# Performance work log

Hardware: AMD Instinct MI355X
Metric: run time of the kernel (lower is better)

The kernel has to match this reference:

```python
import jax, jax.numpy as jnp
import numpy as np

B, L, DIM = 16, 1024, 768
HEADS, DIM_HEAD = 12, 64
INNER = HEADS * DIM_HEAD  # 768


def _make_perm(key, l, dim):
    # first `dim` entries identity, rest a random permutation of [dim, l*dim)
    tail = dim + jax.random.permutation(key, (l - 1) * dim)
    return jnp.concatenate([jnp.arange(dim), tail]).astype(jnp.int32)


def setup_inputs() -> dict:
    key = jax.random.key(0)
    kx, kq, kk, kv, ko, kp1, kp2 = jax.random.split(key, 7)
    s = DIM ** -0.5
    return {
        "x": jax.random.normal(kx, (B, L, DIM), dtype=jnp.float32),
        "Wq": jax.random.normal(kq, (DIM, INNER), dtype=jnp.float32) * s,
        "Wk": jax.random.normal(kk, (DIM, INNER), dtype=jnp.float32) * s,
        "Wv": jax.random.normal(kv, (DIM, INNER), dtype=jnp.float32) * s,
        "Wo": jax.random.normal(ko, (INNER, DIM), dtype=jnp.float32) * (INNER ** -0.5),
        "bo": jnp.zeros((DIM,), dtype=jnp.float32),
        "permq": _make_perm(kp1, L, DIM),
        "permk": _make_perm(kp2, L, DIM),
    }


def reference(x, Wq, Wk, Wv, Wo, bo, permq, permk):
    b, l, d = x.shape
    scale = DIM_HEAD ** -0.5
    flat = x.reshape(b, l * d)
    xq = flat[:, permq].reshape(b, l, d)  # irregular gather across (seq*dim)
    xk = flat[:, permk].reshape(b, l, d)
    # projections + head split: b n (h d) -> b h n d
    q = (xq @ Wq).reshape(b, l, HEADS, DIM_HEAD).transpose(0, 2, 1, 3)
    k = (xk @ Wk).reshape(b, l, HEADS, DIM_HEAD).transpose(0, 2, 1, 3)
    v = (x @ Wv).reshape(b, l, HEADS, DIM_HEAD).transpose(0, 2, 1, 3)
    dots = jnp.einsum('bhnd,bhmd->bhnm', q, k) * scale
    attn = jax.nn.softmax(dots, axis=-1)
    out = jnp.einsum('bhnm,bhmd->bhnd', attn, v)
    out = out.transpose(0, 2, 1, 3).reshape(b, l, INNER)
    return out @ Wo + bo
```

## Files before the change

### kernel.cpp

```cpp
#include <hip/hip_runtime.h>

typedef unsigned short u16;
typedef __attribute__((ext_vector_type(8))) short bf16x8;
typedef __attribute__((ext_vector_type(4))) float f32x4;
typedef __attribute__((ext_vector_type(16))) float f32x16;

#define MFMA16(a, b, c) __builtin_amdgcn_mfma_f32_16x16x32_bf16(a, b, c, 0, 0, 0)
#define MFMA32(a, b, c) __builtin_amdgcn_mfma_f32_32x32x16_bf16(a, b, c, 0, 0, 0)

#if defined(__has_builtin)
# if __has_builtin(__builtin_amdgcn_cvt_pk_bf16_f32)
#  define HAS_CVT_PK 1
# else
#  define HAS_CVT_PK 0
# endif
#else
# define HAS_CVT_PK 0
#endif

__device__ __forceinline__ u16 f2b(float f) {
    union { float f; unsigned int u; } v;
    v.f = f;
    unsigned int u = v.u;
    return (u16)((u + 0x7fffu + ((u >> 16) & 1u)) >> 16);
}

__device__ __forceinline__ unsigned int f2b_pk(float a, float b) {
#if HAS_CVT_PK
    auto r = __builtin_amdgcn_cvt_pk_bf16_f32(a, b);
    unsigned int u;
    __builtin_memcpy(&u, &r, 4);
    return u;
#else
    return (unsigned int)f2b(a) | ((unsigned int)f2b(b) << 16);
#endif
}

__device__ __forceinline__ unsigned int cvtpk_asm(float a, float b) {
    unsigned int r;
    asm("v_cvt_pk_bf16_f32 %0, %1, %2" : "=v"(r) : "v"(a), "v"(b));
    return r;
}

__device__ __forceinline__ void g2l16(const u16* gsrc, u16* ldst) {
    __builtin_amdgcn_global_load_lds(
        (const __attribute__((address_space(1))) void*)gsrc,
        (__attribute__((address_space(3))) void*)ldst,
        16, 0, 0);
}

__global__ __launch_bounds__(256) void prep_weights(
    const float* __restrict__ Wq, const float* __restrict__ Wk,
    const float* __restrict__ Wv, const float* __restrict__ Wo,
    u16* __restrict__ wqt, u16* __restrict__ wkt,
    u16* __restrict__ wvt, u16* __restrict__ wot) {
    int id = blockIdx.x * 256 + threadIdx.x;
    int k = id / 768, n = id % 768;
    int t = n * 768 + k;
    wqt[t] = f2b(Wq[id] * (0.125f * 1.44269504088896340736f));
    wkt[t] = f2b(Wk[id]);
    wvt[t] = f2b(Wv[id]);
    wot[t] = f2b(Wo[id]);
}

__global__ __launch_bounds__(256) void cast_transpose(
    const float* __restrict__ x, u16* __restrict__ xb, u16* __restrict__ xT) {
    __shared__ __attribute__((aligned(16))) u16 T[16 * 1032];
    int t = threadIdx.x;
    int j0 = blockIdx.x * 1024;
#pragma unroll
    for (int b = 0; b < 16; ++b) {
        float4 v = *(const float4*)&x[(size_t)b * 786432 + j0 + 4 * t];
        uint2 o = make_uint2(f2b_pk(v.x, v.y), f2b_pk(v.z, v.w));
        *(uint2*)&T[b * 1032 + 4 * t] = o;
        *(uint2*)&xb[(size_t)b * 786432 + j0 + 4 * t] = o;
    }
    __syncthreads();
#pragma unroll
    for (int p = 0; p < 4; ++p) {
        int jl = t + 256 * p;
        union { u16 u[16]; int4 v[2]; } r;
#pragma unroll
        for (int b = 0; b < 16; ++b) r.u[b] = T[b * 1032 + jl];
        size_t base = (size_t)(j0 + jl) * 16;
        *(int4*)&xT[base] = r.v[0];
        *(int4*)&xT[base + 8] = r.v[1];
    }
}

__global__ __launch_bounds__(256) void gather_rows(
    const u16* __restrict__ xT, const int* __restrict__ permq,
    const int* __restrict__ permk, u16* __restrict__ xqT,
    u16* __restrict__ xkT) {
    int j = blockIdx.x * 256 + threadIdx.x;
    int pq = permq[j], pk = permk[j];
    const int4* sq = (const int4*)&xT[(size_t)pq * 16];
    const int4* sk = (const int4*)&xT[(size_t)pk * 16];
    int4 q0 = sq[0], q1 = sq[1];
    int4 k0 = sk[0], k1 = sk[1];
    int4* dq = (int4*)&xqT[(size_t)j * 16];
    int4* dk = (int4*)&xkT[(size_t)j * 16];
    dq[0] = q0; dq[1] = q1;
    dk[0] = k0; dk[1] = k1;
}

__global__ __launch_bounds__(256) void untranspose(
    const u16* __restrict__ srcQ, const u16* __restrict__ srcK,
    u16* __restrict__ dstQ, u16* __restrict__ dstK) {
    __shared__ u16 T[16 * 1034];
    const u16* src = blockIdx.y ? srcK : srcQ;
    u16* dst = blockIdx.y ? dstK : dstQ;
    int t = threadIdx.x;
    int j0 = blockIdx.x * 1024;
#pragma unroll
    for (int p = 0; p < 8; ++p) {
        int c = p * 256 + t;
        union { u16 u[8]; int4 v; } r;
        r.v = *(const int4*)&src[(size_t)j0 * 16 + c * 8];
        int jl = c >> 1, h = (c & 1) * 8;
#pragma unroll
        for (int w = 0; w < 8; ++w) T[(h + w) * 1034 + jl] = r.u[w];
    }
    __syncthreads();
#pragma unroll
    for (int b = 0; b < 16; ++b) {
        const unsigned int* s = (const unsigned int*)&T[b * 1034 + 4 * t];
        uint2 o = make_uint2(s[0], s[1]);
        *(uint2*)&dst[(size_t)b * 786432 + j0 + 4 * t] = o;
    }
}

__device__ __forceinline__ void gemm_core(
    const u16* __restrict__ A, const u16* __restrict__ Bt,
    u16* __restrict__ Cb, float* __restrict__ Cf,
    const float* __restrict__ bias, int m0, int n0, int K, int N, int mode) {
    __shared__ __attribute__((aligned(16))) u16 As[128 * 64];
    __shared__ __attribute__((aligned(16))) u16 Bs[128 * 64];
    int tid = threadIdx.x;
    int wave = tid >> 6, lane = tid & 63;
    int lo = lane & 15, quad = lane >> 4;
    int wm = (wave >> 1) * 64, wn = (wave & 1) * 64;
    f32x4 acc[4][4] = {};

    const u16* pA[4];
    const u16* pB[4];
    u16* lA[4];
    u16* lB[4];
#pragma unroll
    for (int p = 0; p < 4; ++p) {
        int c = p * 256 + wave * 64 + lane;
        int row = c >> 3;
        int scol = ((c & 7) ^ (row & 7)) * 8;
        pA[p] = A + (size_t)(m0 + row) * K + scol;
        pB[p] = Bt + (size_t)(n0 + row) * K + scol;
        lA[p] = &As[(p * 256 + wave * 64) * 8];
        lB[p] = &Bs[(p * 256 + wave * 64) * 8];
    }

    for (int k0 = 0; k0 < K; k0 += 64) {
        __syncthreads();
#pragma unroll
        for (int p = 0; p < 4; ++p) g2l16(pA[p], lA[p]);
#pragma unroll
        for (int p = 0; p < 4; ++p) g2l16(pB[p], lB[p]);
#pragma unroll
        for (int p = 0; p < 4; ++p) { pA[p] += 64; pB[p] += 64; }
        __syncthreads();
#pragma unroll
        for (int kk = 0; kk < 2; ++kk) {
            bf16x8 af[4], bf[4];
#pragma unroll
            for (int mi = 0; mi < 4; ++mi) {
                int row = wm + mi * 16 + lo;
                af[mi] = *(const bf16x8*)&As[row * 64 + (((kk << 2) | quad) ^ (lo & 7)) * 8];
            }
#pragma unroll
            for (int nj = 0; nj < 4; ++nj) {
                int row = wn + nj * 16 + lo;
                bf[nj] = *(const bf16x8*)&Bs[row * 64 + (((kk << 2) | quad) ^ (lo & 7)) * 8];
            }
#pragma unroll
            for (int mi = 0; mi < 4; ++mi)
#pragma unroll
                for (int nj = 0; nj < 4; ++nj)
                    acc[mi][nj] = MFMA16(af[mi], bf[nj], acc[mi][nj]);
        }
    }
#pragma unroll
    for (int mi = 0; mi < 4; ++mi)
#pragma unroll
        for (int nj = 0; nj < 4; ++nj) {
            int col = n0 + wn + nj * 16 + lo;
#pragma unroll
            for (int r = 0; r < 4; ++r) {
                int row = m0 + wm + mi * 16 + quad * 4 + r;
                float v = acc[mi][nj][r];
                if (mode) Cf[(size_t)row * N + col] = v + bias[col];
                else      Cb[(size_t)row * N + col] = f2b(v);
            }
        }
}

__global__ __launch_bounds__(256) void gemm_qkv(
    const u16* __restrict__ xqb, const u16* __restrict__ wqt, u16* __restrict__ Qb,
    const u16* __restrict__ xkb, const u16* __restrict__ wkt, u16* __restrict__ Kb,
    const u16* __restrict__ xb,  const u16* __restrict__ wvt, u16* __restrict__ Vb) {
    int id = blockIdx.x;
    int xcd = id & 7, slot = id >> 3;
    int gi = slot / 6, j = slot % 6;
    int group = xcd + 8 * gi;
    int my = group & 127, z = group >> 7;
    const u16* A = (z == 0) ? xqb : (z == 1) ? xkb : xb;
    const u16* W = (z == 0) ? wqt : (z == 1) ? wkt : wvt;
    u16* C = (z == 0) ? Qb : (z == 1) ? Kb : Vb;
    gemm_core(A, W, C, nullptr, nullptr, my * 128, j * 128, 768, 768, 0);
}

__global__ __launch_bounds__(256) void gemm_out(
    const u16* __restrict__ A, const u16* __restrict__ Bt,
    float* __restrict__ Cf, const float* __restrict__ bias) {
    int id = blockIdx.x;
    int xcd = id & 7, slot = id >> 3;
    int gi = slot / 6, j = slot % 6;
    int group = xcd + 8 * gi;
    gemm_core(A, Bt, nullptr, Cf, bias, group * 128, j * 128, 768, 768, 1);
}

#define LDA 72
__global__ __launch_bounds__(256) void transpose_v(
    const u16* __restrict__ Vb, u16* __restrict__ Vt) {
    __shared__ __attribute__((aligned(16))) u16 tile[64 * LDA];
    int lt = blockIdx.x;
    int bh = blockIdx.y;
    int b = bh / 12, h = bh % 12;
    int tid = threadIdx.x;
    int row = tid >> 3, co = (tid & 7) * 8;
#pragma unroll
    for (int p = 0; p < 2; ++p) {
        int r2 = row + p * 32;
        *(int4*)&tile[r2 * LDA + co] =
            *(const int4*)&Vb[(size_t)(b * 1024 + lt * 64 + r2) * 768 + h * 64 + co];
    }
    __syncthreads();
    int d = tid >> 2, nc = (tid & 3) * 16;
    union { u16 u[16]; int4 v[2]; } tt;
#pragma unroll
    for (int j = 0; j < 16; ++j)
        tt.u[j] = tile[(nc + j) * LDA + d];
    size_t base = ((size_t)bh * 64 + d) * 1024 + lt * 64 + nc;
    *(int4*)&Vt[base] = tt.v[0];
    *(int4*)&Vt[base + 8] = tt.v[1];
}

#define LDK 72
__global__ __launch_bounds__(256) void flash_attn(
    const u16* __restrict__ Qb, const u16* __restrict__ Kb,
    const u16* __restrict__ Vt, u16* __restrict__ AO) {
    __shared__ __attribute__((aligned(16))) u16 Ks[64 * LDK];
    __shared__ __attribute__((aligned(16))) u16 Vs[64 * LDK];
    int id = blockIdx.x;
    int bh = (id & 7) + ((id >> 6) << 3);
    int qt = (id >> 3) & 7;
    int b = bh / 12, h = bh % 12;
    int tid = threadIdx.x, wave = tid >> 6, lane = tid & 63;
    int ln = lane & 31, hi = lane >> 5;
    int q0 = qt * 128;

    bf16x8 qa[4];
    {
        const u16* qrow = &Qb[(size_t)(b * 1024 + q0 + wave * 32 + ln) * 768 + h * 64 + hi * 8];
#pragma unroll
        for (int kk = 0; kk < 4; ++kk)
            qa[kk] = *(const bf16x8*)&qrow[kk * 16];
    }

    const float M2 = 24.0f;
    float l_own = 0.0f;
    f32x16 acc_o[2] = {};
    const size_t kbase = (size_t)b * 1024 * 768 + h * 64;
    const size_t vbase = (size_t)bh * 64 * 1024;
    int srow = tid >> 3, sco = (tid & 7) * 8;

    int4 kr0 = *(const int4*)&Kb[kbase + (size_t)srow * 768 + sco];
    int4 kr1 = *(const int4*)&Kb[kbase + (size_t)(srow + 32) * 768 + sco];
    int4 vr0 = *(const int4*)&Vt[vbase + (size_t)srow * 1024 + sco];
    int4 vr1 = *(const int4*)&Vt[vbase + (size_t)(srow + 32) * 1024 + sco];

    for (int t = 0; t < 16; ++t) {
        __syncthreads();
        *(int4*)&Ks[srow * LDK + sco] = kr0;
        *(int4*)&Ks[(srow + 32) * LDK + sco] = kr1;
        *(int4*)&Vs[srow * LDK + sco] = vr0;
        *(int4*)&Vs[(srow + 32) * LDK + sco] = vr1;
        __syncthreads();
        int tn = (t + 1) & 15;
        kr0 = *(const int4*)&Kb[kbase + (size_t)(tn * 64 + srow) * 768 + sco];
        kr1 = *(const int4*)&Kb[kbase + (size_t)(tn * 64 + srow + 32) * 768 + sco];
        vr0 = *(const int4*)&Vt[vbase + (size_t)srow * 1024 + tn * 64 + sco];
        vr1 = *(const int4*)&Vt[vbase + (size_t)(srow + 32) * 1024 + tn * 64 + sco];
        f32x16 sacc[2] = {};
#pragma unroll
        for (int nj = 0; nj < 2; ++nj)
#pragma unroll
            for (int kk = 0; kk < 4; ++kk) {
                bf16x8 kb = *(const bf16x8*)&Ks[(ln + 32 * nj) * LDK + kk * 16 + hi * 8];
                sacc[nj] = MFMA32(kb, qa[kk], sacc[nj]);
            }
#pragma unroll
        for (int nj = 0; nj < 2; ++nj) {
            float p[16];
#pragma unroll
            for (int r = 0; r < 16; ++r)
                p[r] = __builtin_amdgcn_exp2f(sacc[nj][r] - M2);
            l_own += (((p[0] + p[1]) + (p[2] + p[3])) + ((p[4] + p[5]) + (p[6] + p[7])))
                   + (((p[8] + p[9]) + (p[10] + p[11])) + ((p[12] + p[13]) + (p[14] + p[15])));
            unsigned int c[8];
#pragma unroll
            for (int m = 0; m < 8; ++m)
                c[m] = cvtpk_asm(p[2 * m], p[2 * m + 1]);
            asm("v_permlane32_swap_b32 %0, %1" : "+v"(c[0]), "+v"(c[2]));
            asm("v_permlane32_swap_b32 %0, %1" : "+v"(c[1]), "+v"(c[3]));
            asm("v_permlane32_swap_b32 %0, %1" : "+v"(c[4]), "+v"(c[6]));
            asm("v_permlane32_swap_b32 %0, %1" : "+v"(c[5]), "+v"(c[7]));
            union { unsigned int w[4]; bf16x8 v; } pa0, pa1;
            pa0.w[0] = c[0]; pa0.w[1] = c[1]; pa0.w[2] = c[2]; pa0.w[3] = c[3];
            pa1.w[0] = c[4]; pa1.w[1] = c[5]; pa1.w[2] = c[6]; pa1.w[3] = c[7];
#pragma unroll
            for (int njd = 0; njd < 2; ++njd) {
                bf16x8 vb0 = *(const bf16x8*)&Vs[(ln + 32 * njd) * LDK + (2 * nj) * 16 + hi * 8];
                acc_o[njd] = MFMA32(pa0.v, vb0, acc_o[njd]);
            }
#pragma unroll
            for (int njd = 0; njd < 2; ++njd) {
                bf16x8 vb1 = *(const bf16x8*)&Vs[(ln + 32 * njd) * LDK + (2 * nj + 1) * 16 + hi * 8];
                acc_o[njd] = MFMA32(pa1.v, vb1, acc_o[njd]);
            }
        }
    }
    float l = l_own + __shfl_xor(l_own, 32, 64);
    float inv = 1.0f / l;
#pragma unroll
    for (int r = 0; r < 16; ++r) {
        int qrow = (r & 3) + 8 * (r >> 2) + 4 * hi;
        float invq = __shfl(inv, qrow, 64);
        int row = b * 1024 + q0 + wave * 32 + qrow;
#pragma unroll
        for (int njd = 0; njd < 2; ++njd)
            AO[(size_t)row * 768 + h * 64 + ln + 32 * njd] = f2b(acc_o[njd][r] * invq);
    }
}

static const size_t SZ_W  = (size_t)768 * 768 * 2;
static const size_t SZ_X  = (size_t)16 * 1024 * 768 * 2;
static const size_t OFF_WQT = 0;
static const size_t OFF_WKT = SZ_W;
static const size_t OFF_WVT = 2 * SZ_W;
static const size_t OFF_WOT = 3 * SZ_W;
static const size_t OFF_XB  = 4 * SZ_W;
static const size_t OFF_XQB = OFF_XB  + SZ_X;
static const size_t OFF_XKB = OFF_XQB + SZ_X;
static const size_t OFF_QB  = OFF_XKB + SZ_X;
static const size_t OFF_KB  = OFF_QB  + SZ_X;
static const size_t OFF_VB  = OFF_KB  + SZ_X;
static const size_t OFF_XT  = OFF_QB;
static const size_t OFF_XQT = OFF_KB;
static const size_t OFF_XKT = OFF_VB;
static const size_t OFF_VT  = OFF_XQB;
static const size_t OFF_AO  = OFF_XKB;

extern "C" void kernel_launch(void* const* d_in, const int* in_sizes, int n_in,
                              void* d_out, int out_size, void* d_ws, size_t ws_size,
                              hipStream_t stream) {
    const float* x  = (const float*)d_in[0];
    const float* Wq = (const float*)d_in[1];
    const float* Wk = (const float*)d_in[2];
    const float* Wv = (const float*)d_in[3];
    const float* Wo = (const float*)d_in[4];
    const float* bo = (const float*)d_in[5];
    const int* permq = (const int*)d_in[6];
    const int* permk = (const int*)d_in[7];
    float* out = (float*)d_out;
    char* ws = (char*)d_ws;
    u16* wqt = (u16*)(ws + OFF_WQT);
    u16* wkt = (u16*)(ws + OFF_WKT);
    u16* wvt = (u16*)(ws + OFF_WVT);
    u16* wot = (u16*)(ws + OFF_WOT);
    u16* xb  = (u16*)(ws + OFF_XB);
    u16* xqb = (u16*)(ws + OFF_XQB);
    u16* xkb = (u16*)(ws + OFF_XKB);
    u16* Qb  = (u16*)(ws + OFF_QB);
    u16* Kb  = (u16*)(ws + OFF_KB);
    u16* Vb  = (u16*)(ws + OFF_VB);
    u16* xT  = (u16*)(ws + OFF_XT);
    u16* xqT = (u16*)(ws + OFF_XQT);
    u16* xkT = (u16*)(ws + OFF_XKT);
    u16* Vt  = (u16*)(ws + OFF_VT);
    u16* AO  = (u16*)(ws + OFF_AO);

    prep_weights<<<2304, 256, 0, stream>>>(Wq, Wk, Wv, Wo, wqt, wkt, wvt, wot);
    cast_transpose<<<768, 256, 0, stream>>>(x, xb, xT);
    gather_rows<<<3072, 256, 0, stream>>>(xT, permq, permk, xqT, xkT);
    untranspose<<<dim3(768, 2), 256, 0, stream>>>(xqT, xkT, xqb, xkb);
    gemm_qkv<<<2304, 256, 0, stream>>>(xqb, wqt, Qb, xkb, wkt, Kb, xb, wvt, Vb);
    transpose_v<<<dim3(16, 192), 256, 0, stream>>>(Vb, Vt);
    flash_attn<<<1536, 256, 0, stream>>>(Qb, Kb, Vt, AO);
    gemm_out<<<768, 256, 0, stream>>>(AO, wot, out, bo);
}
```

Measured before the change: 377.4 us.

## Rewrite GEMM core as 256x256 double-buffered tile with 8 waves

Replaces the 128x128 single-buffered GEMM tile (4 waves) with a 256x256 tile computed by 8 waves, LDS double-buffered so global-to-LDS loads for the next K step are issued interleaved with MFMA work on the current buffer. Raw s_barrier plus setprio are used to keep waves in lockstep and prioritize MFMA issue. The aim is more operand reuse per loaded byte and hiding load latency, at the cost of 128KB LDS per block, many more accumulator registers, and far fewer blocks (576 and 192), which may underfill the 256 CUs, especially for gemm_out.

```diff
diff --git a/kernel.cpp b/kernel.cpp
--- a/kernel.cpp
+++ b/kernel.cpp
@@ -130,100 +130,112 @@
     }
 }
 
-__device__ __forceinline__ void gemm_core(
+__device__ __forceinline__ void gemm256_core(
     const u16* __restrict__ A, const u16* __restrict__ Bt,
     u16* __restrict__ Cb, float* __restrict__ Cf,
     const float* __restrict__ bias, int m0, int n0, int K, int N, int mode) {
-    __shared__ __attribute__((aligned(16))) u16 As[128 * 64];
-    __shared__ __attribute__((aligned(16))) u16 Bs[128 * 64];
+    __shared__ __attribute__((aligned(16))) u16 As[2][256 * 64];
+    __shared__ __attribute__((aligned(16))) u16 Bs[2][256 * 64];
     int tid = threadIdx.x;
     int wave = tid >> 6, lane = tid & 63;
+    int wr = wave >> 2, wc = wave & 3;
     int lo = lane & 15, quad = lane >> 4;
-    int wm = (wave >> 1) * 64, wn = (wave & 1) * 64;
-    f32x4 acc[4][4] = {};
-
-    const u16* pA[4];
-    const u16* pB[4];
-    u16* lA[4];
-    u16* lB[4];
-#pragma unroll
-    for (int p = 0; p < 4; ++p) {
-        int c = p * 256 + wave * 64 + lane;
-        int row = c >> 3;
-        int scol = ((c & 7) ^ (row & 7)) * 8;
-        pA[p] = A + (size_t)(m0 + row) * K + scol;
-        pB[p] = Bt + (size_t)(n0 + row) * K + scol;
-        lA[p] = &As[(p * 256 + wave * 64) * 8];
-        lB[p] = &Bs[(p * 256 + wave * 64) * 8];
-    }
-
-    for (int k0 = 0; k0 < K; k0 += 64) {
-        __syncthreads();
-#pragma unroll
-        for (int p = 0; p < 4; ++p) g2l16(pA[p], lA[p]);
-#pragma unroll
-        for (int p = 0; p < 4; ++p) g2l16(pB[p], lB[p]);
-#pragma unroll
-        for (int p = 0; p < 4; ++p) { pA[p] += 64; pB[p] += 64; }
-        __syncthreads();
-#pragma unroll
-        for (int kk = 0; kk < 2; ++kk) {
+    f32x4 acc[8][4] = {};
+
+    const u16* Ab = A + (size_t)m0 * K;
+    const u16* Bb = Bt + (size_t)n0 * K;
+    int r_off = wave * 8 + (lane >> 3);
+    int s_off = ((lane & 7) ^ (lane >> 3)) * 8;
+
+#pragma unroll
+    for (int h = 0; h < 2; ++h)
+#pragma unroll
+        for (int i = 0; i < 2; ++i) {
+            g2l16(Ab + (size_t)(h * 128 + i * 64 + r_off) * K + s_off,
+                  &As[0][(h * 128 + i * 64 + wave * 8) * 64]);
+            g2l16(Bb + (size_t)(h * 128 + i * 64 + r_off) * K + s_off,
+                  &Bs[0][(h * 128 + i * 64 + wave * 8) * 64]);
+        }
+    asm volatile("s_waitcnt vmcnt(0)" ::: "memory");
+    __builtin_amdgcn_s_barrier();
+
+    const int NT = K >> 6;
+    for (int s = 0; s < NT; ++s) {
+        int cur = s & 1, nxt = cur ^ 1;
+        int kn = (s + 1) << 6;
+        const bool more = (s + 1 < NT);
+#pragma unroll
+        for (int q = 0; q < 4; ++q) {
+            const int ks = q >> 1, qm = q & 1;
+            int fs = ((ks * 4 + quad) ^ (lo & 7)) * 8;
             bf16x8 af[4], bf[4];
 #pragma unroll
-            for (int mi = 0; mi < 4; ++mi) {
-                int row = wm + mi * 16 + lo;
-                af[mi] = *(const bf16x8*)&As[row * 64 + (((kk << 2) | quad) ^ (lo & 7)) * 8];
+            for (int mi = 0; mi < 4; ++mi)
+                af[mi] = *(const bf16x8*)&As[cur][(wr * 128 + (qm * 4 + mi) * 16 + lo) * 64 + fs];
+#pragma unroll
+            for (int nj = 0; nj < 4; ++nj)
+                bf[nj] = *(const bf16x8*)&Bs[cur][(wc * 64 + nj * 16 + lo) * 64 + fs];
+            if (more) {
+                const u16* src = (q < 2) ? Ab : Bb;
+                u16* dst = (q < 2) ? &As[nxt][0] : &Bs[nxt][0];
+                const int h = q & 1;
+                g2l16(src + (size_t)(h * 128 + r_off) * K + kn + s_off,
+                      dst + (h * 128 + wave * 8) * 64);
+                g2l16(src + (size_t)(h * 128 + 64 + r_off) * K + kn + s_off,
+                      dst + (h * 128 + 64 + wave * 8) * 64);
             }
-#pragma unroll
-            for (int nj = 0; nj < 4; ++nj) {
-                int row = wn + nj * 16 + lo;
-                bf[nj] = *(const bf16x8*)&Bs[row * 64 + (((kk << 2) | quad) ^ (lo & 7)) * 8];
-            }
+            __builtin_amdgcn_s_barrier();
+            __builtin_amdgcn_s_setprio(1);
 #pragma unroll
             for (int mi = 0; mi < 4; ++mi)
 #pragma unroll
                 for (int nj = 0; nj < 4; ++nj)
-                    acc[mi][nj] = MFMA16(af[mi], bf[nj], acc[mi][nj]);
+                    acc[qm * 4 + mi][nj] = MFMA16(af[mi], bf[nj], acc[qm * 4 + mi][nj]);
+            __builtin_amdgcn_s_setprio(0);
+            if (q < 3) __builtin_amdgcn_s_barrier();
         }
-    }
-#pragma unroll
-    for (int mi = 0; mi < 4; ++mi)
+        asm volatile("s_waitcnt vmcnt(0)" ::: "memory");
+        __builtin_amdgcn_s_barrier();
+    }
+
+#pragma unroll
+    for (int mf = 0; mf < 8; ++mf)
 #pragma unroll
         for (int nj = 0; nj < 4; ++nj) {
-            int col = n0 + wn + nj * 16 + lo;
+            int col = n0 + wc * 64 + nj * 16 + lo;
 #pragma unroll
             for (int r = 0; r < 4; ++r) {
-                int row = m0 + wm + mi * 16 + quad * 4 + r;
-                float v = acc[mi][nj][r];
+                int row = m0 + wr * 128 + mf * 16 + quad * 4 + r;
+                float v = acc[mf][nj][r];
                 if (mode) Cf[(size_t)row * N + col] = v + bias[col];
                 else      Cb[(size_t)row * N + col] = f2b(v);
             }
         }
 }
 
-__global__ __launch_bounds__(256) void gemm_qkv(
+__global__ __launch_bounds__(512, 2) void gemm_qkv(
     const u16* __restrict__ xqb, const u16* __restrict__ wqt, u16* __restrict__ Qb,
     const u16* __restrict__ xkb, const u16* __restrict__ wkt, u16* __restrict__ Kb,
     const u16* __restrict__ xb,  const u16* __restrict__ wvt, u16* __restrict__ Vb) {
     int id = blockIdx.x;
     int xcd = id & 7, slot = id >> 3;
-    int gi = slot / 6, j = slot % 6;
+    int gi = slot / 3, j = slot % 3;
     int group = xcd + 8 * gi;
-    int my = group & 127, z = group >> 7;
+    int my = group & 63, z = group >> 6;
     const u16* A = (z == 0) ? xqb : (z == 1) ? xkb : xb;
     const u16* W = (z == 0) ? wqt : (z == 1) ? wkt : wvt;
     u16* C = (z == 0) ? Qb : (z == 1) ? Kb : Vb;
-    gemm_core(A, W, C, nullptr, nullptr, my * 128, j * 128, 768, 768, 0);
-}
-
-__global__ __launch_bounds__(256) void gemm_out(
+    gemm256_core(A, W, C, nullptr, nullptr, my * 256, j * 256, 768, 768, 0);
+}
+
+__global__ __launch_bounds__(512, 2) void gemm_out(
     const u16* __restrict__ A, const u16* __restrict__ Bt,
     float* __restrict__ Cf, const float* __restrict__ bias) {
     int id = blockIdx.x;
     int xcd = id & 7, slot = id >> 3;
-    int gi = slot / 6, j = slot % 6;
+    int gi = slot / 3, j = slot % 3;
     int group = xcd + 8 * gi;
-    gemm_core(A, Bt, nullptr, Cf, bias, group * 128, j * 128, 768, 768, 1);
+    gemm256_core(A, Bt, nullptr, Cf, bias, group * 256, j * 256, 768, 768, 1);
 }
 
 #define LDA 72
@@ -401,8 +413,8 @@
     cast_transpose<<<768, 256, 0, stream>>>(x, xb, xT);
     gather_rows<<<3072, 256, 0, stream>>>(xT, permq, permk, xqT, xkT);
     untranspose<<<dim3(768, 2), 256, 0, stream>>>(xqT, xkT, xqb, xkb);
-    gemm_qkv<<<2304, 256, 0, stream>>>(xqb, wqt, Qb, xkb, wkt, Kb, xb, wvt, Vb);
+    gemm_qkv<<<576, 512, 0, stream>>>(xqb, wqt, Qb, xkb, wkt, Kb, xb, wvt, Vb);
     transpose_v<<<dim3(16, 192), 256, 0, stream>>>(Vb, Vt);
     flash_attn<<<1536, 256, 0, stream>>>(Qb, Kb, Vt, AO);
-    gemm_out<<<768, 256, 0, stream>>>(AO, wot, out, bo);
-}
+    gemm_out<<<192, 512, 0, stream>>>(AO, wot, out, bo);
+}
```

Measured after the change: 386.2 us. +2.3%, slower.
